# Performance work log

Hardware: AMD Instinct MI355X
Metric: run time of the kernel (lower is better)

The kernel has to match this reference:

```python
import jax, jax.numpy as jnp
import numpy as np

C, P, PQ, D, B, HW = 32, 64, 4, 2048, 256, 7
N = HW * HW  # 49 spatial positions


def _bn(x, g, b):
    # eval-mode BatchNorm2d with running_mean=0, running_var=1
    s = g / jnp.sqrt(1.0 + 1e-5)
    return x * s[None, :, None, None] + b[None, :, None, None]


def _g1x1(x, w):
    # grouped 1x1 conv: x [B, C*pin, H, W], w [C, pout, pin]
    Bs, _, Hh, Ww = x.shape
    xg = x.reshape(Bs, C, w.shape[2], Hh, Ww)
    y = jnp.einsum('bcihw,coi->bcohw', xg, w)
    return y.reshape(Bs, C * w.shape[1], Hh, Ww)


def setup_inputs() -> dict:
    key = jax.random.key(0)
    ks = iter(jax.random.split(key, 40))
    def rn(shape, s=1.0):
        return jax.random.normal(next(ks), shape, jnp.float32) * s
    inp = {
        'x': rn((B, D, HW, HW)),
        'W1': rn((C * P, D), 0.02), 'g1': 1.0 + rn((C * P,), 0.1), 'b1': rn((C * P,), 0.1),
        'W2': rn((C * P, P, 3, 3), 0.04), 'g2': 1.0 + rn((C * P,), 0.1), 'b2': rn((C * P,), 0.1),
        'Wq': rn((C, PQ, P), 0.1), 'gq': 1.0 + rn((C * PQ,), 0.1), 'bq': rn((C * PQ,), 0.1),
        'Wk': rn((C, PQ, P), 0.1), 'gk': 1.0 + rn((C * PQ,), 0.1), 'bk': rn((C * PQ,), 0.1),
        'Wout': rn((C, PQ, P), 0.1), 'gout': 1.0 + rn((C * PQ,), 0.1), 'bout': rn((C * PQ,), 0.1),
        'Wcr': rn((C, C, PQ), 0.1), 'gcr': 1.0 + rn((C * C,), 0.1), 'bcr': rn((C * C,), 0.1),
        'gcr1': 1.0 + rn((C * PQ,), 0.1), 'bcr1': rn((C * PQ,), 0.1),
        'Wa': rn((C, P, PQ), 0.1), 'ba': rn((C * P,), 0.1),
        'Wb': rn((C, P, PQ), 0.1), 'bb': rn((C * P,), 0.1),
        'W3': rn((D, C * P), 0.02), 'g3': 1.0 + rn((D,), 0.1), 'b3': rn((D,), 0.1),
    }
    return inp


def reference(x, W1, g1, b1, W2, g2, b2, Wq, gq, bq, Wk, gk, bk,
              Wout, gout, bout, Wcr, gcr, bcr, gcr1, bcr1,
              Wa, ba, Wb, bb, W3, g3, b3):
    # stem: 1x1 conv + BN, grouped 3x3 conv + BN
    Xc = _bn(jnp.einsum('bdhw,ed->behw', x, W1), g1, b1)             # [B,2048,7,7]
    Zc = _bn(jax.lax.conv_general_dilated(
        Xc, W2, (1, 1), 'SAME', feature_group_count=C,
        dimension_numbers=('NCHW', 'OIHW', 'NCHW')), g2, b2)         # [B,2048,7,7]

    # channel self-attention: per-group q(1xp_) @ k(p_xN)
    pooled = jnp.mean(Zc, axis=(2, 3), keepdims=True)                # AvgPool2d(7) -> 1x1
    q = _bn(_g1x1(pooled, Wq), gq, bq).reshape(-1, C, PQ)            # [B,c,p_]
    k = _bn(_g1x1(Zc, Wk), gk, bk).reshape(-1, C, PQ, N)             # [B,c,p_,N]
    scores = jnp.einsum('bcp,bcpn->bcn', q, k)                       # [B,c,N]
    # torch Softmax2d on 3D [B,1,N] normalizes dim -3 == batch dim (faithful quirk)
    M = jax.nn.softmax(scores, axis=0)                               # [B,c,N]

    Zg = Zc.reshape(-1, C, P, N)
    zout = jnp.einsum('bcpn,bcn->bcp', Zg, M).reshape(-1, C * P, 1, 1)
    hc = _bn(_g1x1(zout, Wout), gout, bout)                          # [B,128,1,1]

    # channel-relation: A [B,c,c] mixes H [B,c,p_]
    A = jnp.tanh(_bn(_g1x1(hc, Wcr), gcr, bcr)).reshape(-1, C, C)
    A = jnp.swapaxes(A, 1, 2)                                        # chunk/cat transpose
    Hm = hc.reshape(-1, C, PQ)                                       # [B,c,p_]
    mix = jnp.matmul(A, Hm) + Hm                                     # [B,c,p_]
    hc_ = jax.nn.relu(_bn(mix.reshape(-1, C * PQ, 1, 1), gcr1, bcr1)).reshape(-1, C, PQ)

    # broadcast back to spatial via attention maps
    M_ = M / jnp.max(M)
    Mchc = jnp.einsum('bcp,bcn->bcpn', hc_, M_).reshape(-1, C * PQ, HW, HW)

    alpha = _g1x1(Mchc, Wa) + ba[None, :, None, None]                # [B,2048,7,7]
    beta = _g1x1(Mchc, Wb) + bb[None, :, None, None]
    Xc_ = jax.nn.relu(Zc * alpha + beta)
    cm = Zc * Xc_

    OUT = _bn(jnp.einsum('behw,de->bdhw', cm, W3), g3, b3)
    return OUT + x
```

## Files before the change

kernel.cpp:

```cpp
#include <hip/hip_runtime.h>
#include <hip/hip_bf16.h>
#include <stdint.h>

#define DI __device__ __forceinline__

typedef __attribute__((ext_vector_type(8))) short short8;
typedef __attribute__((ext_vector_type(4))) float floatx4;

DI float bf2f(short u) {
  union { unsigned int i; float f; } v;
  v.i = ((unsigned int)(unsigned short)u) << 16;
  return v.f;
}
DI short f2bf(float f) {
  union { float f; unsigned int i; } v; v.f = f;
  unsigned int r = v.i + 0x7FFFu + ((v.i >> 16) & 1u);
  return (short)(r >> 16);
}

DI void gload16(const void* g, void* l) {
  __builtin_amdgcn_global_load_lds(
      (const __attribute__((address_space(1))) void*)g,
      (__attribute__((address_space(3))) void*)l,
      16, 0, 0);
}

__global__ __launch_bounds__(256) void k_cvt(const float* __restrict__ src,
                                             short* __restrict__ dst, int n) {
  int i = blockIdx.x * 256 + threadIdx.x;
  if (i < n) dst[i] = f2bf(src[i]);
}

__global__ __launch_bounds__(256) void k_w2r(const float* __restrict__ W2,
                                             short* __restrict__ W2R) {
  int idx = blockIdx.x * 256 + threadIdx.x;
  if (idx >= 32 * 9 * 64 * 64) return;
  int pi = idx & 63;
  int po = (idx >> 6) & 63;
  int ct = idx >> 12;
  int tap = ct % 9, c = ct / 9;
  W2R[idx] = f2bf(W2[((c * 64 + po) * 64 + pi) * 9 + tap]);
}

__global__ __launch_bounds__(256) void k_xt(const float* __restrict__ x,
                                            short* __restrict__ xT) {
  __shared__ float tile[64 * 49];
  int b = blockIdx.x, dc = blockIdx.y;
  const float* xp = x + ((size_t)b * 2048 + dc * 64) * 49;
  for (int i = threadIdx.x; i < 64 * 49; i += 256) tile[i] = xp[i];
  __syncthreads();
  for (int i = threadIdx.x; i < 64 * 49; i += 256) {
    int n = i >> 6, dl = i & 63;
    xT[((size_t)(b * 49 + n)) * 2048 + dc * 64 + dl] = f2bf(tile[dl * 49 + n]);
  }
}

__global__ __launch_bounds__(256) void k_gemm1(
    const short* __restrict__ xT, const short* __restrict__ W1b,
    const float* __restrict__ g1, const float* __restrict__ b1,
    short* __restrict__ XcPad) {
  __shared__ __attribute__((aligned(16))) short As[128 * 32];
  __shared__ __attribute__((aligned(16))) short Bs[128 * 32];
  const int tid = threadIdx.x;
  const int wave = tid >> 6, lane = tid & 63;
  const int mt = blockIdx.x, et = blockIdx.y;
  const int srow = tid >> 2, schunk = tid & 3;
  const short* asrc0 = xT + (size_t)(mt * 128 + srow) * 2048 + schunk * 8;
  const short* asrc1 = asrc0 + (size_t)64 * 2048;
  const short* bsrc0 = W1b + (size_t)(et * 128 + srow) * 2048 + schunk * 8;
  const short* bsrc1 = bsrc0 + (size_t)64 * 2048;
  short* alds0 = &As[wave * 16 * 32];
  short* alds1 = &As[(64 + wave * 16) * 32];
  short* blds0 = &Bs[wave * 16 * 32];
  short* blds1 = &Bs[(64 + wave * 16) * 32];
  const int wr = wave >> 1, wc = wave & 1;
  const int aoff = (wr * 64 + (lane & 15)) * 32 + (lane >> 4) * 8;
  const int boff = (wc * 64 + (lane & 15)) * 32 + (lane >> 4) * 8;
  floatx4 acc[4][4] = {};
  for (int kt = 0; kt < 64; ++kt) {
    const int ko = kt * 32;
    gload16(asrc0 + ko, alds0);
    gload16(asrc1 + ko, alds1);
    gload16(bsrc0 + ko, blds0);
    gload16(bsrc1 + ko, blds1);
    __syncthreads();
    short8 a[4], b[4];
#pragma unroll
    for (int i = 0; i < 4; ++i) a[i] = *(const short8*)&As[aoff + i * 16 * 32];
#pragma unroll
    for (int j = 0; j < 4; ++j) b[j] = *(const short8*)&Bs[boff + j * 16 * 32];
#pragma unroll
    for (int i = 0; i < 4; ++i)
#pragma unroll
      for (int j = 0; j < 4; ++j)
        acc[i][j] = __builtin_amdgcn_mfma_f32_16x16x32_bf16(a[i], b[j], acc[i][j], 0, 0, 0);
    __syncthreads();
  }
  const float rs = rsqrtf(1.0f + 1e-5f);
  size_t abase[16];
#pragma unroll
  for (int i = 0; i < 4; ++i)
#pragma unroll
    for (int r = 0; r < 4; ++r) {
      int m = mt * 128 + wr * 64 + i * 16 + (lane >> 4) * 4 + r;
      int bb = m / 49, n = m % 49, h = n / 7, w = n % 7;
      abase[i * 4 + r] = ((size_t)bb * 81 + (h + 1) * 9 + (w + 1)) * 2048;
    }
#pragma unroll
  for (int j = 0; j < 4; ++j) {
    int e = et * 128 + wc * 64 + j * 16 + (lane & 15);
    float s = g1[e] * rs, bo = b1[e];
#pragma unroll
    for (int i = 0; i < 4; ++i)
#pragma unroll
      for (int r = 0; r < 4; ++r)
        XcPad[abase[i * 4 + r] + e] = f2bf(acc[i][j][r] * s + bo);
  }
}

__global__ __launch_bounds__(256) void k_conv(
    const short* __restrict__ XcPad, const short* __restrict__ W2R,
    const float* __restrict__ g2, const float* __restrict__ b2,
    short* __restrict__ ZcT) {
  __shared__ __attribute__((aligned(16))) short As[128 * 32];
  __shared__ __attribute__((aligned(16))) short Bs[64 * 32];
  const int tid = threadIdx.x;
  const int wave = tid >> 6, lane = tid & 63;
  const int mt = blockIdx.x, c = blockIdx.y;
  const int srow = tid >> 2, schunk = tid & 3;
  int m0 = mt * 128 + srow;
  int b0 = m0 / 49, n0 = m0 % 49, h0 = n0 / 7, w0 = n0 % 7;
  int m1 = m0 + 64;
  int b1v = m1 / 49, n1 = m1 % 49, h1 = n1 / 7, w1 = n1 % 7;
  const short* abase = XcPad + (size_t)c * 64 + schunk * 8;
  const short* wbase = W2R + (size_t)c * 9 * 4096 + srow * 64 + schunk * 8;
  short* alds0 = &As[wave * 16 * 32];
  short* alds1 = &As[(64 + wave * 16) * 32];
  short* blds = &Bs[wave * 16 * 32];
  const int wr = wave >> 1, wc = wave & 1;
  const int aoff = (wr * 64 + (lane & 15)) * 32 + (lane >> 4) * 8;
  const int boff = (wc * 32 + (lane & 15)) * 32 + (lane >> 4) * 8;
  floatx4 acc[4][2] = {};
  for (int tap = 0; tap < 9; ++tap) {
    const int dy = tap / 3, dx = tap % 3;
    const size_t r0 = ((size_t)b0 * 81 + (h0 + dy) * 9 + (w0 + dx)) * 2048;
    const size_t r1 = ((size_t)b1v * 81 + (h1 + dy) * 9 + (w1 + dx)) * 2048;
#pragma unroll
    for (int kk = 0; kk < 2; ++kk) {
      gload16(abase + r0 + kk * 32, alds0);
      gload16(abase + r1 + kk * 32, alds1);
      gload16(wbase + tap * 4096 + kk * 32, blds);
      __syncthreads();
      short8 a[4], b[2];
#pragma unroll
      for (int i = 0; i < 4; ++i) a[i] = *(const short8*)&As[aoff + i * 16 * 32];
#pragma unroll
      for (int j = 0; j < 2; ++j) b[j] = *(const short8*)&Bs[boff + j * 16 * 32];
#pragma unroll
      for (int i = 0; i < 4; ++i)
#pragma unroll
        for (int j = 0; j < 2; ++j)
          acc[i][j] = __builtin_amdgcn_mfma_f32_16x16x32_bf16(a[i], b[j], acc[i][j], 0, 0, 0);
      __syncthreads();
    }
  }
  const float rs = rsqrtf(1.0f + 1e-5f);
#pragma unroll
  for (int j = 0; j < 2; ++j) {
    int e = c * 64 + wc * 32 + j * 16 + (lane & 15);
    float s = g2[e] * rs, bo = b2[e];
#pragma unroll
    for (int i = 0; i < 4; ++i)
#pragma unroll
      for (int r = 0; r < 4; ++r) {
        int m = mt * 128 + wr * 64 + i * 16 + (lane >> 4) * 4 + r;
        ZcT[(size_t)m * 2048 + e] = f2bf(acc[i][j][r] * s + bo);
      }
  }
}

__global__ __launch_bounds__(256) void k_pool(const short* __restrict__ ZcT,
                                              float* __restrict__ pooled) {
  int b = blockIdx.x;
  for (int e = threadIdx.x; e < 2048; e += 256) {
    float s = 0.f;
    for (int n = 0; n < 49; ++n) s += bf2f(ZcT[((size_t)(b * 49 + n)) * 2048 + e]);
    pooled[b * 2048 + e] = s * (1.0f / 49.0f);
  }
}

__global__ __launch_bounds__(128) void k_q(const float* __restrict__ pooled,
                                           const float* __restrict__ Wq,
                                           const float* __restrict__ gq,
                                           const float* __restrict__ bq,
                                           float* __restrict__ qb) {
  int b = blockIdx.x, t = threadIdx.x;
  int c = t >> 2;
  float s = 0.f;
  for (int pi = 0; pi < 64; ++pi) s += Wq[t * 64 + pi] * pooled[b * 2048 + c * 64 + pi];
  const float rs = rsqrtf(1.0f + 1e-5f);
  qb[b * 128 + t] = s * gq[t] * rs + bq[t];
}

__global__ __launch_bounds__(256) void k_scores(
    const short* __restrict__ ZcT, const float* __restrict__ Wk,
    const float* __restrict__ gk, const float* __restrict__ bk,
    const float* __restrict__ qb, float* __restrict__ scores) {
  int b = blockIdx.x;
  const float rs = rsqrtf(1.0f + 1e-5f);
  for (int idx = threadIdx.x; idx < 1568; idx += 256) {
    int c = idx / 49, n = idx % 49;
    float acc[4] = {0.f, 0.f, 0.f, 0.f};
    const short* z = &ZcT[((size_t)(b * 49 + n)) * 2048 + c * 64];
    for (int pi = 0; pi < 64; ++pi) {
      float zv = bf2f(z[pi]);
#pragma unroll
      for (int pq = 0; pq < 4; ++pq) acc[pq] += Wk[(c * 4 + pq) * 64 + pi] * zv;
    }
    float sc = 0.f;
#pragma unroll
    for (int pq = 0; pq < 4; ++pq) {
      float kv = acc[pq] * gk[c * 4 + pq] * rs + bk[c * 4 + pq];
      sc += qb[b * 128 + c * 4 + pq] * kv;
    }
    scores[b * 1568 + idx] = sc;
  }
}

__global__ __launch_bounds__(256) void k_softmax(const float* __restrict__ scores,
                                                 float* __restrict__ Msm,
                                                 unsigned int* __restrict__ maxM) {
  int cn = blockIdx.x, t = threadIdx.x;
  float v = scores[t * 1568 + cn];
  __shared__ float red[4], red2[4];
  float m = v;
#pragma unroll
  for (int o = 1; o < 64; o <<= 1) m = fmaxf(m, __shfl_xor(m, o));
  if ((t & 63) == 0) red[t >> 6] = m;
  __syncthreads();
  m = fmaxf(fmaxf(red[0], red[1]), fmaxf(red[2], red[3]));
  float e = expf(v - m);
  float s = e;
#pragma unroll
  for (int o = 1; o < 64; o <<= 1) s += __shfl_xor(s, o);
  if ((t & 63) == 0) red2[t >> 6] = s;
  __syncthreads();
  s = red2[0] + red2[1] + red2[2] + red2[3];
  Msm[t * 1568 + cn] = e / s;
  if (t == 0) atomicMax(maxM, __float_as_uint(1.0f / s));
}

__global__ __launch_bounds__(256) void k_tail(
    const short* __restrict__ ZcT, const float* __restrict__ Msm,
    const float* __restrict__ Wout, const float* __restrict__ gout,
    const float* __restrict__ bout, const float* __restrict__ Wcr,
    const float* __restrict__ gcr, const float* __restrict__ bcr,
    const float* __restrict__ gcr1, const float* __restrict__ bcr1,
    const float* __restrict__ Wa, const float* __restrict__ Wb,
    float* __restrict__ va, float* __restrict__ vb) {
  int b = blockIdx.x, t = threadIdx.x;
  __shared__ float Mrow[1568];
  __shared__ float zout[2048];
  __shared__ float hcl[128];
  __shared__ float tb[1024];
  __shared__ float hcp[128];
  const float rs = rsqrtf(1.0f + 1e-5f);
  for (int i = t; i < 1568; i += 256) Mrow[i] = Msm[b * 1568 + i];
  __syncthreads();
  for (int e = t; e < 2048; e += 256) {
    int c = e >> 6;
    float s = 0.f;
    for (int n = 0; n < 49; ++n)
      s += bf2f(ZcT[((size_t)(b * 49 + n)) * 2048 + e]) * Mrow[c * 49 + n];
    zout[e] = s;
  }
  __syncthreads();
  if (t < 128) {
    int c = t >> 2;
    float s = 0.f;
    for (int p = 0; p < 64; ++p) s += Wout[t * 64 + p] * zout[c * 64 + p];
    hcl[t] = s * gout[t] * rs + bout[t];
  }
  __syncthreads();
  for (int i = t; i < 1024; i += 256) {
    int c = i >> 5;
    float s = 0.f;
#pragma unroll
    for (int k = 0; k < 4; ++k) s += Wcr[i * 4 + k] * hcl[c * 4 + k];
    tb[i] = tanhf(s * gcr[i] * rs + bcr[i]);
  }
  __syncthreads();
  if (t < 128) {
    int i = t >> 2, pq = t & 3;
    float s = hcl[t];
    for (int j = 0; j < 32; ++j) s += tb[j * 32 + i] * hcl[j * 4 + pq];
    hcp[t] = fmaxf(s * gcr1[t] * rs + bcr1[t], 0.0f);
  }
  __syncthreads();
  for (int e = t; e < 2048; e += 256) {
    int c = e >> 6;
    float sa = 0.f, sb = 0.f;
#pragma unroll
    for (int pq = 0; pq < 4; ++pq) {
      float h = hcp[c * 4 + pq];
      sa += Wa[e * 4 + pq] * h;
      sb += Wb[e * 4 + pq] * h;
    }
    va[b * 2048 + e] = sa;
    vb[b * 2048 + e] = sb;
  }
}

__global__ __launch_bounds__(256) void k_cm(
    const short* __restrict__ ZcT, const float* __restrict__ Msm,
    const unsigned int* __restrict__ maxM, const float* __restrict__ va,
    const float* __restrict__ vb, const float* __restrict__ ba,
    const float* __restrict__ bb, short* __restrict__ cm) {
  int m = blockIdx.x;
  int b = m / 49, n = m % 49;
  __shared__ float Minv[32];
  if (threadIdx.x < 32) {
    float mx = __uint_as_float(*maxM);
    Minv[threadIdx.x] = Msm[b * 1568 + threadIdx.x * 49 + n] / mx;
  }
  __syncthreads();
  for (int e = threadIdx.x; e < 2048; e += 256) {
    float zc = bf2f(ZcT[(size_t)m * 2048 + e]);
    int c = e >> 6;
    float al = va[b * 2048 + e] * Minv[c] + ba[e];
    float bt = vb[b * 2048 + e] * Minv[c] + bb[e];
    float xc = fmaxf(zc * al + bt, 0.0f);
    cm[(size_t)m * 2048 + e] = f2bf(zc * xc);
  }
}

__global__ __launch_bounds__(256) void k_gemm2(
    const short* __restrict__ W3b, const short* __restrict__ cm,
    const float* __restrict__ g3, const float* __restrict__ b3,
    const float* __restrict__ x, float* __restrict__ out) {
  __shared__ __attribute__((aligned(16))) short As[128 * 32];
  __shared__ __attribute__((aligned(16))) short Bs[128 * 32];
  const int tid = threadIdx.x;
  const int wave = tid >> 6, lane = tid & 63;
  const int mt = blockIdx.x;
  const int dt = blockIdx.y;
  const int srow = tid >> 2, schunk = tid & 3;
  const short* asrc0 = W3b + (size_t)(dt * 128 + srow) * 2048 + schunk * 8;
  const short* asrc1 = asrc0 + (size_t)64 * 2048;
  const short* bsrc0 = cm + (size_t)(mt * 128 + srow) * 2048 + schunk * 8;
  const short* bsrc1 = bsrc0 + (size_t)64 * 2048;
  short* alds0 = &As[wave * 16 * 32];
  short* alds1 = &As[(64 + wave * 16) * 32];
  short* blds0 = &Bs[wave * 16 * 32];
  short* blds1 = &Bs[(64 + wave * 16) * 32];
  const int wr = wave >> 1, wc = wave & 1;
  const int aoff = (wr * 64 + (lane & 15)) * 32 + (lane >> 4) * 8;
  const int boff = (wc * 64 + (lane & 15)) * 32 + (lane >> 4) * 8;
  floatx4 acc[4][4] = {};
  for (int kt = 0; kt < 64; ++kt) {
    const int ko = kt * 32;
    gload16(asrc0 + ko, alds0);
    gload16(asrc1 + ko, alds1);
    gload16(bsrc0 + ko, blds0);
    gload16(bsrc1 + ko, blds1);
    __syncthreads();
    short8 a[4], b[4];
#pragma unroll
    for (int i = 0; i < 4; ++i) a[i] = *(const short8*)&As[aoff + i * 16 * 32];
#pragma unroll
    for (int j = 0; j < 4; ++j) b[j] = *(const short8*)&Bs[boff + j * 16 * 32];
#pragma unroll
    for (int i = 0; i < 4; ++i)
#pragma unroll
      for (int j = 0; j < 4; ++j)
        acc[i][j] = __builtin_amdgcn_mfma_f32_16x16x32_bf16(a[i], b[j], acc[i][j], 0, 0, 0);
    __syncthreads();
  }
  const float rs = rsqrtf(1.0f + 1e-5f);
  size_t cbb[4];
#pragma unroll
  for (int j = 0; j < 4; ++j) {
    int m = mt * 128 + wc * 64 + j * 16 + (lane & 15);
    int bb = m / 49, n = m % 49;
    cbb[j] = (size_t)bb * (2048 * 49) + n;
  }
#pragma unroll
  for (int i = 0; i < 4; ++i)
#pragma unroll
    for (int r = 0; r < 4; ++r) {
      int d = dt * 128 + wr * 64 + i * 16 + (lane >> 4) * 4 + r;
      float s = g3[d] * rs, bo = b3[d];
      size_t dterm = (size_t)d * 49;
#pragma unroll
      for (int j = 0; j < 4; ++j) {
        size_t adr = cbb[j] + dterm;
        out[adr] = acc[i][j][r] * s + bo + x[adr];
      }
    }
}

extern "C" void kernel_launch(void* const* d_in, const int* in_sizes, int n_in,
                              void* d_out, int out_size, void* d_ws, size_t ws_size,
                              hipStream_t stream) {
  (void)in_sizes; (void)n_in; (void)out_size; (void)ws_size;
  const float* x    = (const float*)d_in[0];
  const float* W1   = (const float*)d_in[1];
  const float* g1   = (const float*)d_in[2];
  const float* b1   = (const float*)d_in[3];
  const float* W2   = (const float*)d_in[4];
  const float* g2   = (const float*)d_in[5];
  const float* b2   = (const float*)d_in[6];
  const float* Wq   = (const float*)d_in[7];
  const float* gq   = (const float*)d_in[8];
  const float* bq   = (const float*)d_in[9];
  const float* Wk   = (const float*)d_in[10];
  const float* gk   = (const float*)d_in[11];
  const float* bk   = (const float*)d_in[12];
  const float* Wout = (const float*)d_in[13];
  const float* gout = (const float*)d_in[14];
  const float* bout = (const float*)d_in[15];
  const float* Wcr  = (const float*)d_in[16];
  const float* gcr  = (const float*)d_in[17];
  const float* bcr  = (const float*)d_in[18];
  const float* gcr1 = (const float*)d_in[19];
  const float* bcr1 = (const float*)d_in[20];
  const float* Wa   = (const float*)d_in[21];
  const float* ba   = (const float*)d_in[22];
  const float* Wb   = (const float*)d_in[23];
  const float* bb   = (const float*)d_in[24];
  const float* W3   = (const float*)d_in[25];
  const float* g3   = (const float*)d_in[26];
  const float* b3   = (const float*)d_in[27];
  float* out = (float*)d_out;

  char* ws = (char*)d_ws;
  short* XcPad  = (short*)(ws + 0);
  short* xT     = (short*)(ws + 84934656);
  short* ZcT    = (short*)(ws + 136314880);
  short* W1b    = (short*)(ws + 187695104);
  short* W3b    = (short*)(ws + 196083712);
  short* W2R    = (short*)(ws + 204472320);
  float* pooled = (float*)(ws + 206831616);
  float* qb     = (float*)(ws + 208928768);
  float* scores = (float*)(ws + 209059840);
  float* Msm    = (float*)(ws + 210665472);
  float* va     = (float*)(ws + 212271104);
  float* vb     = (float*)(ws + 214368256);
  unsigned int* maxM = (unsigned int*)(ws + 216465408);
  short* cm = xT;

  hipMemsetAsync(XcPad, 0, 84934656, stream);
  hipMemsetAsync(maxM, 0, 4, stream);

  k_cvt<<<16384, 256, 0, stream>>>(W1, W1b, 4194304);
  k_cvt<<<16384, 256, 0, stream>>>(W3, W3b, 4194304);
  k_w2r<<<4608, 256, 0, stream>>>(W2, W2R);
  k_xt<<<dim3(256, 32), 256, 0, stream>>>(x, xT);
  k_gemm1<<<dim3(98, 16), 256, 0, stream>>>(xT, W1b, g1, b1, XcPad);
  k_conv<<<dim3(98, 32), 256, 0, stream>>>(XcPad, W2R, g2, b2, ZcT);
  k_pool<<<256, 256, 0, stream>>>(ZcT, pooled);
  k_q<<<256, 128, 0, stream>>>(pooled, Wq, gq, bq, qb);
  k_scores<<<256, 256, 0, stream>>>(ZcT, Wk, gk, bk, qb, scores);
  k_softmax<<<1568, 256, 0, stream>>>(scores, Msm, maxM);
  k_tail<<<256, 256, 0, stream>>>(ZcT, Msm, Wout, gout, bout, Wcr, gcr, bcr,
                                  gcr1, bcr1, Wa, Wb, va, vb);
  k_cm<<<12544, 256, 0, stream>>>(ZcT, Msm, maxM, va, vb, ba, bb, cm);
  k_gemm2<<<dim3(98, 16), 256, 0, stream>>>(W3b, cm, g3, b3, x, out);
}
```

Before: 969.5 us.

## Double-buffer GEMM/conv LDS loads, swizzle block order, fuse pool/q/scores, vectorize cm

The two GEMMs and the grouped conv now stage global-to-LDS loads into a second buffer while the MFMAs run on the first, which halves the barriers per k-step and lets load latency overlap with compute. They also launch on a 1D grid with an XCD-aware swizzle so neighbouring tiles share cache. The pooling, q projection and score kernels are merged into one kernel that keeps pooled and q in shared memory. The cm kernel and the score inner loop now use 8-wide bf16 vector loads. The cost is twice the LDS per block and more code complexity.

```diff
diff --git a/kernel.cpp b/kernel.cpp
--- a/kernel.cpp
+++ b/kernel.cpp
@@ -59,43 +59,56 @@
     const short* __restrict__ xT, const short* __restrict__ W1b,
     const float* __restrict__ g1, const float* __restrict__ b1,
     short* __restrict__ XcPad) {
-  __shared__ __attribute__((aligned(16))) short As[128 * 32];
-  __shared__ __attribute__((aligned(16))) short Bs[128 * 32];
+  __shared__ __attribute__((aligned(16))) short As[2][4096];
+  __shared__ __attribute__((aligned(16))) short Bs[2][4096];
   const int tid = threadIdx.x;
   const int wave = tid >> 6, lane = tid & 63;
-  const int mt = blockIdx.x, et = blockIdx.y;
+  const int wg = blockIdx.x;
+  const int swz = (wg & 7) * 196 + (wg >> 3);
+  const int mt = swz >> 4, et = swz & 15;
   const int srow = tid >> 2, schunk = tid & 3;
   const short* asrc0 = xT + (size_t)(mt * 128 + srow) * 2048 + schunk * 8;
   const short* asrc1 = asrc0 + (size_t)64 * 2048;
   const short* bsrc0 = W1b + (size_t)(et * 128 + srow) * 2048 + schunk * 8;
   const short* bsrc1 = bsrc0 + (size_t)64 * 2048;
-  short* alds0 = &As[wave * 16 * 32];
-  short* alds1 = &As[(64 + wave * 16) * 32];
-  short* blds0 = &Bs[wave * 16 * 32];
-  short* blds1 = &Bs[(64 + wave * 16) * 32];
   const int wr = wave >> 1, wc = wave & 1;
   const int aoff = (wr * 64 + (lane & 15)) * 32 + (lane >> 4) * 8;
   const int boff = (wc * 64 + (lane & 15)) * 32 + (lane >> 4) * 8;
   floatx4 acc[4][4] = {};
-  for (int kt = 0; kt < 64; ++kt) {
+  auto STAGE = [&](int buf, int kt) {
     const int ko = kt * 32;
-    gload16(asrc0 + ko, alds0);
-    gload16(asrc1 + ko, alds1);
-    gload16(bsrc0 + ko, blds0);
-    gload16(bsrc1 + ko, blds1);
-    __syncthreads();
+    gload16(asrc0 + ko, &As[buf][wave * 512]);
+    gload16(asrc1 + ko, &As[buf][2048 + wave * 512]);
+    gload16(bsrc0 + ko, &Bs[buf][wave * 512]);
+    gload16(bsrc1 + ko, &Bs[buf][2048 + wave * 512]);
+  };
+  auto COMPUTE = [&](int buf) {
     short8 a[4], b[4];
 #pragma unroll
-    for (int i = 0; i < 4; ++i) a[i] = *(const short8*)&As[aoff + i * 16 * 32];
-#pragma unroll
-    for (int j = 0; j < 4; ++j) b[j] = *(const short8*)&Bs[boff + j * 16 * 32];
+    for (int i = 0; i < 4; ++i) a[i] = *(const short8*)&As[buf][aoff + i * 512];
+#pragma unroll
+    for (int j = 0; j < 4; ++j) b[j] = *(const short8*)&Bs[buf][boff + j * 512];
 #pragma unroll
     for (int i = 0; i < 4; ++i)
 #pragma unroll
       for (int j = 0; j < 4; ++j)
         acc[i][j] = __builtin_amdgcn_mfma_f32_16x16x32_bf16(a[i], b[j], acc[i][j], 0, 0, 0);
+  };
+  STAGE(0, 0);
+  __syncthreads();
+#pragma unroll 1
+  for (int kt = 0; kt < 62; kt += 2) {
+    STAGE(1, kt + 1);
+    COMPUTE(0);
     __syncthreads();
-  }
+    STAGE(0, kt + 2);
+    COMPUTE(1);
+    __syncthreads();
+  }
+  STAGE(1, 63);
+  COMPUTE(0);
+  __syncthreads();
+  COMPUTE(1);
   const float rs = rsqrtf(1.0f + 1e-5f);
   size_t abase[16];
 #pragma unroll
@@ -122,48 +135,60 @@
     const short* __restrict__ XcPad, const short* __restrict__ W2R,
     const float* __restrict__ g2, const float* __restrict__ b2,
     short* __restrict__ ZcT) {
-  __shared__ __attribute__((aligned(16))) short As[128 * 32];
-  __shared__ __attribute__((aligned(16))) short Bs[64 * 32];
+  __shared__ __attribute__((aligned(16))) short As[2][4096];
+  __shared__ __attribute__((aligned(16))) short Bs[2][2048];
   const int tid = threadIdx.x;
   const int wave = tid >> 6, lane = tid & 63;
-  const int mt = blockIdx.x, c = blockIdx.y;
+  const int wg = blockIdx.x;
+  const int swz = (wg & 7) * 392 + (wg >> 3);
+  const int mt = swz >> 5, c = swz & 31;
   const int srow = tid >> 2, schunk = tid & 3;
   int m0 = mt * 128 + srow;
   int b0 = m0 / 49, n0 = m0 % 49, h0 = n0 / 7, w0 = n0 % 7;
   int m1 = m0 + 64;
   int b1v = m1 / 49, n1 = m1 % 49, h1 = n1 / 7, w1 = n1 % 7;
+  const size_t base0 = ((size_t)b0 * 81 + (h0 + 1) * 9 + (w0 + 1)) * 2048;
+  const size_t base1 = ((size_t)b1v * 81 + (h1 + 1) * 9 + (w1 + 1)) * 2048;
   const short* abase = XcPad + (size_t)c * 64 + schunk * 8;
   const short* wbase = W2R + (size_t)c * 9 * 4096 + srow * 64 + schunk * 8;
-  short* alds0 = &As[wave * 16 * 32];
-  short* alds1 = &As[(64 + wave * 16) * 32];
-  short* blds = &Bs[wave * 16 * 32];
   const int wr = wave >> 1, wc = wave & 1;
   const int aoff = (wr * 64 + (lane & 15)) * 32 + (lane >> 4) * 8;
   const int boff = (wc * 32 + (lane & 15)) * 32 + (lane >> 4) * 8;
   floatx4 acc[4][2] = {};
-  for (int tap = 0; tap < 9; ++tap) {
-    const int dy = tap / 3, dx = tap % 3;
-    const size_t r0 = ((size_t)b0 * 81 + (h0 + dy) * 9 + (w0 + dx)) * 2048;
-    const size_t r1 = ((size_t)b1v * 81 + (h1 + dy) * 9 + (w1 + dx)) * 2048;
-#pragma unroll
-    for (int kk = 0; kk < 2; ++kk) {
-      gload16(abase + r0 + kk * 32, alds0);
-      gload16(abase + r1 + kk * 32, alds1);
-      gload16(wbase + tap * 4096 + kk * 32, blds);
-      __syncthreads();
-      short8 a[4], b[2];
-#pragma unroll
-      for (int i = 0; i < 4; ++i) a[i] = *(const short8*)&As[aoff + i * 16 * 32];
-#pragma unroll
-      for (int j = 0; j < 2; ++j) b[j] = *(const short8*)&Bs[boff + j * 16 * 32];
-#pragma unroll
-      for (int i = 0; i < 4; ++i)
-#pragma unroll
-        for (int j = 0; j < 2; ++j)
-          acc[i][j] = __builtin_amdgcn_mfma_f32_16x16x32_bf16(a[i], b[j], acc[i][j], 0, 0, 0);
-      __syncthreads();
-    }
-  }
+  auto CSTAGE = [&](int buf, int s) {
+    const int tap = s >> 1, kk = s & 1;
+    const int toff = ((tap / 3 - 1) * 9 + (tap % 3 - 1)) * 2048;
+    gload16(abase + base0 + toff + kk * 32, &As[buf][wave * 512]);
+    gload16(abase + base1 + toff + kk * 32, &As[buf][2048 + wave * 512]);
+    gload16(wbase + tap * 4096 + kk * 32, &Bs[buf][wave * 512]);
+  };
+  auto CCOMPUTE = [&](int buf) {
+    short8 a[4], b[2];
+#pragma unroll
+    for (int i = 0; i < 4; ++i) a[i] = *(const short8*)&As[buf][aoff + i * 512];
+#pragma unroll
+    for (int j = 0; j < 2; ++j) b[j] = *(const short8*)&Bs[buf][boff + j * 512];
+#pragma unroll
+    for (int i = 0; i < 4; ++i)
+#pragma unroll
+      for (int j = 0; j < 2; ++j)
+        acc[i][j] = __builtin_amdgcn_mfma_f32_16x16x32_bf16(a[i], b[j], acc[i][j], 0, 0, 0);
+  };
+  CSTAGE(0, 0);
+  __syncthreads();
+#pragma unroll 1
+  for (int s = 0; s < 16; s += 2) {
+    CSTAGE(1, s + 1);
+    CCOMPUTE(0);
+    __syncthreads();
+    CSTAGE(0, s + 2);
+    CCOMPUTE(1);
+    __syncthreads();
+  }
+  CSTAGE(1, 17);
+  CCOMPUTE(0);
+  __syncthreads();
+  CCOMPUTE(1);
   const float rs = rsqrtf(1.0f + 1e-5f);
 #pragma unroll
   for (int j = 0; j < 2; ++j) {
@@ -179,49 +204,48 @@
   }
 }
 
-__global__ __launch_bounds__(256) void k_pool(const short* __restrict__ ZcT,
-                                              float* __restrict__ pooled) {
-  int b = blockIdx.x;
-  for (int e = threadIdx.x; e < 2048; e += 256) {
+__global__ __launch_bounds__(256) void k_scores(
+    const short* __restrict__ ZcT, const float* __restrict__ Wq,
+    const float* __restrict__ gq, const float* __restrict__ bq,
+    const float* __restrict__ Wk, const float* __restrict__ gk,
+    const float* __restrict__ bk, float* __restrict__ scores) {
+  int b = blockIdx.x, t = threadIdx.x;
+  __shared__ float pooled[2048];
+  __shared__ float qv[128];
+  const float rs = rsqrtf(1.0f + 1e-5f);
+  for (int e = t; e < 2048; e += 256) {
     float s = 0.f;
     for (int n = 0; n < 49; ++n) s += bf2f(ZcT[((size_t)(b * 49 + n)) * 2048 + e]);
-    pooled[b * 2048 + e] = s * (1.0f / 49.0f);
-  }
-}
-
-__global__ __launch_bounds__(128) void k_q(const float* __restrict__ pooled,
-                                           const float* __restrict__ Wq,
-                                           const float* __restrict__ gq,
-                                           const float* __restrict__ bq,
-                                           float* __restrict__ qb) {
-  int b = blockIdx.x, t = threadIdx.x;
-  int c = t >> 2;
-  float s = 0.f;
-  for (int pi = 0; pi < 64; ++pi) s += Wq[t * 64 + pi] * pooled[b * 2048 + c * 64 + pi];
-  const float rs = rsqrtf(1.0f + 1e-5f);
-  qb[b * 128 + t] = s * gq[t] * rs + bq[t];
-}
-
-__global__ __launch_bounds__(256) void k_scores(
-    const short* __restrict__ ZcT, const float* __restrict__ Wk,
-    const float* __restrict__ gk, const float* __restrict__ bk,
-    const float* __restrict__ qb, float* __restrict__ scores) {
-  int b = blockIdx.x;
-  const float rs = rsqrtf(1.0f + 1e-5f);
-  for (int idx = threadIdx.x; idx < 1568; idx += 256) {
+    pooled[e] = s * (1.0f / 49.0f);
+  }
+  __syncthreads();
+  if (t < 128) {
+    int c = t >> 2;
+    float s = 0.f;
+    for (int pi = 0; pi < 64; ++pi) s += Wq[t * 64 + pi] * pooled[c * 64 + pi];
+    qv[t] = s * gq[t] * rs + bq[t];
+  }
+  __syncthreads();
+  for (int idx = t; idx < 1568; idx += 256) {
     int c = idx / 49, n = idx % 49;
+    const short8* z = (const short8*)&ZcT[((size_t)(b * 49 + n)) * 2048 + c * 64];
     float acc[4] = {0.f, 0.f, 0.f, 0.f};
-    const short* z = &ZcT[((size_t)(b * 49 + n)) * 2048 + c * 64];
-    for (int pi = 0; pi < 64; ++pi) {
-      float zv = bf2f(z[pi]);
-#pragma unroll
-      for (int pq = 0; pq < 4; ++pq) acc[pq] += Wk[(c * 4 + pq) * 64 + pi] * zv;
+#pragma unroll
+    for (int p8 = 0; p8 < 8; ++p8) {
+      short8 v = z[p8];
+#pragma unroll
+      for (int j = 0; j < 8; ++j) {
+        float zv = bf2f(v[j]);
+#pragma unroll
+        for (int pq = 0; pq < 4; ++pq)
+          acc[pq] += Wk[(c * 4 + pq) * 64 + p8 * 8 + j] * zv;
+      }
     }
     float sc = 0.f;
 #pragma unroll
     for (int pq = 0; pq < 4; ++pq) {
       float kv = acc[pq] * gk[c * 4 + pq] * rs + bk[c * 4 + pq];
-      sc += qb[b * 128 + c * 4 + pq] * kv;
+      sc += qv[c * 4 + pq] * kv;
     }
     scores[b * 1568 + idx] = sc;
   }
@@ -324,58 +348,75 @@
     Minv[threadIdx.x] = Msm[b * 1568 + threadIdx.x * 49 + n] / mx;
   }
   __syncthreads();
-  for (int e = threadIdx.x; e < 2048; e += 256) {
-    float zc = bf2f(ZcT[(size_t)m * 2048 + e]);
-    int c = e >> 6;
-    float al = va[b * 2048 + e] * Minv[c] + ba[e];
-    float bt = vb[b * 2048 + e] * Minv[c] + bb[e];
+  const int e0 = threadIdx.x * 8;
+  short8 z8 = *(const short8*)&ZcT[(size_t)m * 2048 + e0];
+  const float mi = Minv[e0 >> 6];
+  short8 o;
+#pragma unroll
+  for (int j = 0; j < 8; ++j) {
+    float zc = bf2f(z8[j]);
+    float al = va[b * 2048 + e0 + j] * mi + ba[e0 + j];
+    float bt = vb[b * 2048 + e0 + j] * mi + bb[e0 + j];
     float xc = fmaxf(zc * al + bt, 0.0f);
-    cm[(size_t)m * 2048 + e] = f2bf(zc * xc);
-  }
+    o[j] = f2bf(zc * xc);
+  }
+  *(short8*)&cm[(size_t)m * 2048 + e0] = o;
 }
 
 __global__ __launch_bounds__(256) void k_gemm2(
     const short* __restrict__ W3b, const short* __restrict__ cm,
     const float* __restrict__ g3, const float* __restrict__ b3,
     const float* __restrict__ x, float* __restrict__ out) {
-  __shared__ __attribute__((aligned(16))) short As[128 * 32];
-  __shared__ __attribute__((aligned(16))) short Bs[128 * 32];
+  __shared__ __attribute__((aligned(16))) short As[2][4096];
+  __shared__ __attribute__((aligned(16))) short Bs[2][4096];
   const int tid = threadIdx.x;
   const int wave = tid >> 6, lane = tid & 63;
-  const int mt = blockIdx.x;
-  const int dt = blockIdx.y;
+  const int wg = blockIdx.x;
+  const int swz = (wg & 7) * 196 + (wg >> 3);
+  const int mt = swz >> 4, dt = swz & 15;
   const int srow = tid >> 2, schunk = tid & 3;
   const short* asrc0 = W3b + (size_t)(dt * 128 + srow) * 2048 + schunk * 8;
   const short* asrc1 = asrc0 + (size_t)64 * 2048;
   const short* bsrc0 = cm + (size_t)(mt * 128 + srow) * 2048 + schunk * 8;
   const short* bsrc1 = bsrc0 + (size_t)64 * 2048;
-  short* alds0 = &As[wave * 16 * 32];
-  short* alds1 = &As[(64 + wave * 16) * 32];
-  short* blds0 = &Bs[wave * 16 * 32];
-  short* blds1 = &Bs[(64 + wave * 16) * 32];
   const int wr = wave >> 1, wc = wave & 1;
   const int aoff = (wr * 64 + (lane & 15)) * 32 + (lane >> 4) * 8;
   const int boff = (wc * 64 + (lane & 15)) * 32 + (lane >> 4) * 8;
   floatx4 acc[4][4] = {};
-  for (int kt = 0; kt < 64; ++kt) {
+  auto STAGE = [&](int buf, int kt) {
     const int ko = kt * 32;
-    gload16(asrc0 + ko, alds0);
-    gload16(asrc1 + ko, alds1);
-    gload16(bsrc0 + ko, blds0);
-    gload16(bsrc1 + ko, blds1);
-    __syncthreads();
+    gload16(asrc0 + ko, &As[buf][wave * 512]);
+    gload16(asrc1 + ko, &As[buf][2048 + wave * 512]);
+    gload16(bsrc0 + ko, &Bs[buf][wave * 512]);
+    gload16(bsrc1 + ko, &Bs[buf][2048 + wave * 512]);
+  };
+  auto COMPUTE = [&](int buf) {
     short8 a[4], b[4];
 #pragma unroll
-    for (int i = 0; i < 4; ++i) a[i] = *(const short8*)&As[aoff + i * 16 * 32];
-#pragma unroll
-    for (int j = 0; j < 4; ++j) b[j] = *(const short8*)&Bs[boff + j * 16 * 32];
+    for (int i = 0; i < 4; ++i) a[i] = *(const short8*)&As[buf][aoff + i * 512];
+#pragma unroll
+    for (int j = 0; j < 4; ++j) b[j] = *(const short8*)&Bs[buf][boff + j * 512];
 #pragma unroll
     for (int i = 0; i < 4; ++i)
 #pragma unroll
       for (int j = 0; j < 4; ++j)
         acc[i][j] = __builtin_amdgcn_mfma_f32_16x16x32_bf16(a[i], b[j], acc[i][j], 0, 0, 0);
+  };
+  STAGE(0, 0);
+  __syncthreads();
+#pragma unroll 1
+  for (int kt = 0; kt < 62; kt += 2) {
+    STAGE(1, kt + 1);
+    COMPUTE(0);
     __syncthreads();
-  }
+    STAGE(0, kt + 2);
+    COMPUTE(1);
+    __syncthreads();
+  }
+  STAGE(1, 63);
+  COMPUTE(0);
+  __syncthreads();
+  COMPUTE(1);
   const float rs = rsqrtf(1.0f + 1e-5f);
   size_t cbb[4];
 #pragma unroll
@@ -440,7 +481,6 @@
   short* W1b    = (short*)(ws + 187695104);
   short* W3b    = (short*)(ws + 196083712);
   short* W2R    = (short*)(ws + 204472320);
-  float* pooled = (float*)(ws + 206831616);
   float* qb     = (float*)(ws + 208928768);
   float* scores = (float*)(ws + 209059840);
   float* Msm    = (float*)(ws + 210665472);
@@ -448,6 +488,7 @@
   float* vb     = (float*)(ws + 214368256);
   unsigned int* maxM = (unsigned int*)(ws + 216465408);
   short* cm = xT;
+  (void)qb;
 
   hipMemsetAsync(XcPad, 0, 84934656, stream);
   hipMemsetAsync(maxM, 0, 4, stream);
@@ -456,14 +497,12 @@
   k_cvt<<<16384, 256, 0, stream>>>(W3, W3b, 4194304);
   k_w2r<<<4608, 256, 0, stream>>>(W2, W2R);
   k_xt<<<dim3(256, 32), 256, 0, stream>>>(x, xT);
-  k_gemm1<<<dim3(98, 16), 256, 0, stream>>>(xT, W1b, g1, b1, XcPad);
-  k_conv<<<dim3(98, 32), 256, 0, stream>>>(XcPad, W2R, g2, b2, ZcT);
-  k_pool<<<256, 256, 0, stream>>>(ZcT, pooled);
-  k_q<<<256, 128, 0, stream>>>(pooled, Wq, gq, bq, qb);
-  k_scores<<<256, 256, 0, stream>>>(ZcT, Wk, gk, bk, qb, scores);
+  k_gemm1<<<1568, 256, 0, stream>>>(xT, W1b, g1, b1, XcPad);
+  k_conv<<<3136, 256, 0, stream>>>(XcPad, W2R, g2, b2, ZcT);
+  k_scores<<<256, 256, 0, stream>>>(ZcT, Wq, gq, bq, Wk, gk, bk, scores);
   k_softmax<<<1568, 256, 0, stream>>>(scores, Msm, maxM);
   k_tail<<<256, 256, 0, stream>>>(ZcT, Msm, Wout, gout, bout, Wcr, gcr, bcr,
                                   gcr1, bcr1, Wa, Wb, va, vb);
   k_cm<<<12544, 256, 0, stream>>>(ZcT, Msm, maxM, va, vb, ba, bb, cm);
-  k_gemm2<<<dim3(98, 16), 256, 0, stream>>>(W3b, cm, g3, b3, x, out);
-}
+  k_gemm2<<<1568, 256, 0, stream>>>(W3b, cm, g3, b3, x, out);
+}
```

New measurement: 1.065 ms. 1.1x slower.
